# Performance work log

Measured on AMD Instinct MI355X. Metric: run time of the kernel, lower is better.

The kernel has to match this reference:

```python
import jax, jax.numpy as jnp
import numpy as np

B, S, H = 32, 4096, 512


def setup_inputs() -> dict:
    key = jax.random.key(0)
    k1, k2, k3, k4, k5 = jax.random.split(key, 5)
    scale = 1.0 / np.sqrt(H)
    return {
        "query": jax.random.normal(k1, (B, H), dtype=jnp.float32),
        "keys": jax.random.normal(k2, (B, S, H), dtype=jnp.float32),
        "key_mask": jnp.ones((B, S), dtype=bool),
        "Wq": jax.random.uniform(k3, (H, H), jnp.float32, -scale, scale),
        "Wk": jax.random.uniform(k4, (H, H), jnp.float32, -scale, scale),
        "v": jax.random.uniform(k5, (H,), jnp.float32, -scale, scale),
    }


def reference(query, keys, key_mask, Wq, Wk, v):
    # Additive (Bahdanau) attention.
    # nn.Linear(x) = x @ W.T
    q = query @ Wq.T                       # [B, H]
    k = keys @ Wk.T                        # [B, S, H]
    scores = jnp.einsum('bsh,h->bs', jnp.tanh(q[:, None, :] + k), v)  # [B, S]
    scores = jnp.where(key_mask, scores, -1e9)
    attn = jax.nn.softmax(scores, axis=-1)  # [B, S]
    ctx = jnp.einsum('bs,bsh->bh', attn, keys)  # [B, H]
    return (ctx, attn)
```

## Files before the change

kernel.cpp:

```cpp
#include <hip/hip_runtime.h>
#include <hip/hip_bf16.h>
#include <cstdint>

#define B_ 32
#define S_ 4096
#define H_ 512

typedef _Float16 f16x8 __attribute__((ext_vector_type(8)));
typedef _Float16 f16x4 __attribute__((ext_vector_type(4)));
typedef float    f32x4 __attribute__((ext_vector_type(4)));

#define GLDS16(gsrc, ldst) \
    __builtin_amdgcn_global_load_lds((const __attribute__((address_space(1))) void*)(gsrc), \
        (__attribute__((address_space(3))) void*)(ldst), 16, 0, 0)

__device__ __forceinline__ float tanh_fast(float x) {
    float e = __expf(2.0f * x);
    return 1.0f - 2.0f / (e + 1.0f);
}

__global__ void prep_q(const float* __restrict__ query,
                       const float* __restrict__ Wq,
                       float* __restrict__ q_ws) {
    int blk = blockIdx.x;
    int b   = blk >> 3;
    int r0  = (blk & 7) * 64;
    int t   = threadIdx.x;
    __shared__ float qs[H_];
    qs[t]       = query[b * H_ + t];
    qs[t + 256] = query[b * H_ + t + 256];
    __syncthreads();
    int row  = r0 + (t >> 2);
    int part = t & 3;
    const float4* wrow = (const float4*)(Wq + (size_t)row * H_) + part * 32;
    const float*  qsp  = qs + part * 128;
    float acc = 0.f;
    #pragma unroll 8
    for (int j = 0; j < 32; ++j) {
        float4 w = wrow[j];
        acc += qsp[j*4+0]*w.x + qsp[j*4+1]*w.y + qsp[j*4+2]*w.z + qsp[j*4+3]*w.w;
    }
    acc += __shfl_xor(acc, 1);
    acc += __shfl_xor(acc, 2);
    if (part == 0) q_ws[b * H_ + row] = acc;
}

__global__ void prep_wk(const float* __restrict__ Wk, _Float16* __restrict__ wk16) {
    int tid = blockIdx.x * 256 + threadIdx.x;
    int c  = tid & 3;
    int i  = (tid >> 2) & 511;
    int ks = tid >> 11;
    const float* src = Wk + (size_t)i * H_ + ks * 32 + c * 8;
    float4 a = *(const float4*)(src);
    float4 d = *(const float4*)(src + 4);
    f16x8 p;
    p[0] = (_Float16)a.x; p[1] = (_Float16)a.y; p[2] = (_Float16)a.z; p[3] = (_Float16)a.w;
    p[4] = (_Float16)d.x; p[5] = (_Float16)d.y; p[6] = (_Float16)d.z; p[7] = (_Float16)d.w;
    int swz = c ^ ((i >> 1) & 3);
    *(f16x8*)(wk16 + (size_t)ks * 16384 + i * 32 + swz * 8) = p;
}

__global__ __launch_bounds__(256, 2) void scores_kernel(
        const float* __restrict__ keys, const _Float16* __restrict__ wk16,
        const float* __restrict__ q_ws, const float* __restrict__ v,
        float* __restrict__ scores) {
    __shared__ __align__(16) _Float16 As[2][64 * 32];
    __shared__ __align__(16) _Float16 Bs[2][512 * 32];
    __shared__ float srow[4][64];

    int t    = threadIdx.x;
    int lane = t & 63;
    int wid  = t >> 6;
    int m0   = blockIdx.x * 64;
    int b    = m0 >> 12;
    const float* akeys = keys + (size_t)m0 * H_;

    f32x4 acc[4][8] = {};

    int arow0 = t >> 3, ac4 = t & 7;
    int arow1 = arow0 + 32;
    int aswz0 = (ac4 >> 1) ^ ((arow0 >> 1) & 3);
    int aswz1 = (ac4 >> 1) ^ ((arow1 >> 1) & 3);

    {
        const _Float16* bsrc = wk16;
        #pragma unroll
        for (int j = 0; j < 8; ++j)
            GLDS16(bsrc + (j * 256 + t) * 8, &Bs[0][(j * 256 + t) * 8]);
        float4 kv0 = *(const float4*)(akeys + (size_t)arow0 * H_ + ac4 * 4);
        float4 kv1 = *(const float4*)(akeys + (size_t)arow1 * H_ + ac4 * 4);
        f16x4 h0, h1;
        h0[0] = (_Float16)kv0.x; h0[1] = (_Float16)kv0.y; h0[2] = (_Float16)kv0.z; h0[3] = (_Float16)kv0.w;
        h1[0] = (_Float16)kv1.x; h1[1] = (_Float16)kv1.y; h1[2] = (_Float16)kv1.z; h1[3] = (_Float16)kv1.w;
        *(f16x4*)&As[0][arow0 * 32 + aswz0 * 8 + (ac4 & 1) * 4] = h0;
        *(f16x4*)&As[0][arow1 * 32 + aswz1 * 8 + (ac4 & 1) * 4] = h1;
    }
    __syncthreads();

    int cur = 0;
    for (int ks = 0; ks < 16; ++ks) {
        int nb = cur ^ 1;
        float4 kv0, kv1;
        if (ks < 15) {
            const _Float16* bsrc = wk16 + (size_t)(ks + 1) * 16384;
            #pragma unroll
            for (int j = 0; j < 8; ++j)
                GLDS16(bsrc + (j * 256 + t) * 8, &Bs[nb][(j * 256 + t) * 8]);
            kv0 = *(const float4*)(akeys + (size_t)arow0 * H_ + (ks + 1) * 32 + ac4 * 4);
            kv1 = *(const float4*)(akeys + (size_t)arow1 * H_ + (ks + 1) * 32 + ac4 * 4);
        }
        int chunk = lane >> 4;
        f16x8 af[4];
        #pragma unroll
        for (int mf = 0; mf < 4; ++mf) {
            int row = mf * 16 + (lane & 15);
            af[mf] = *(const f16x8*)&As[cur][row * 32 + (chunk ^ ((row >> 1) & 3)) * 8];
        }
        f16x8 bf[8];
        #pragma unroll
        for (int nf = 0; nf < 8; ++nf) {
            int row = wid * 128 + nf * 16 + (lane & 15);
            bf[nf] = *(const f16x8*)&Bs[cur][row * 32 + (chunk ^ ((row >> 1) & 3)) * 8];
        }
        #pragma unroll
        for (int mf = 0; mf < 4; ++mf)
            #pragma unroll
            for (int nf = 0; nf < 8; ++nf)
                acc[mf][nf] = __builtin_amdgcn_mfma_f32_16x16x32_f16(af[mf], bf[nf], acc[mf][nf], 0, 0, 0);
        if (ks < 15) {
            f16x4 h0, h1;
            h0[0] = (_Float16)kv0.x; h0[1] = (_Float16)kv0.y; h0[2] = (_Float16)kv0.z; h0[3] = (_Float16)kv0.w;
            h1[0] = (_Float16)kv1.x; h1[1] = (_Float16)kv1.y; h1[2] = (_Float16)kv1.z; h1[3] = (_Float16)kv1.w;
            *(f16x4*)&As[nb][arow0 * 32 + aswz0 * 8 + (ac4 & 1) * 4] = h0;
            *(f16x4*)&As[nb][arow1 * 32 + aswz1 * 8 + (ac4 & 1) * 4] = h1;
        }
        __syncthreads();
        cur = nb;
    }

    float qv[8], vv[8];
    #pragma unroll
    for (int nf = 0; nf < 8; ++nf) {
        int col = wid * 128 + nf * 16 + (lane & 15);
        qv[nf] = q_ws[b * H_ + col];
        vv[nf] = v[col];
    }
    #pragma unroll
    for (int mf = 0; mf < 4; ++mf) {
        f32x4 rs = {0.f, 0.f, 0.f, 0.f};
        #pragma unroll
        for (int nf = 0; nf < 8; ++nf)
            #pragma unroll
            for (int r = 0; r < 4; ++r)
                rs[r] += tanh_fast(qv[nf] + acc[mf][nf][r]) * vv[nf];
        #pragma unroll
        for (int off = 1; off < 16; off <<= 1)
            #pragma unroll
            for (int r = 0; r < 4; ++r)
                rs[r] += __shfl_xor(rs[r], off);
        if ((lane & 15) == 0) {
            #pragma unroll
            for (int r = 0; r < 4; ++r)
                srow[wid][mf * 16 + (lane >> 4) * 4 + r] = rs[r];
        }
    }
    __syncthreads();
    if (t < 64)
        scores[m0 + t] = srow[0][t] + srow[1][t] + srow[2][t] + srow[3][t];
}

__global__ void softmax_kernel(const float* __restrict__ scores,
                               const int* __restrict__ mask,
                               float* __restrict__ attn) {
    int b = blockIdx.x, t = threadIdx.x;
    __shared__ float red[8];
    float x[16];
    float m = -1e30f;
    #pragma unroll
    for (int j = 0; j < 16; ++j) {
        int s = t + j * 256;
        float sc = scores[b * S_ + s];
        x[j] = (mask[b * S_ + s] != 0) ? sc : -1e9f;
        m = fmaxf(m, x[j]);
    }
    #pragma unroll
    for (int off = 1; off < 64; off <<= 1) m = fmaxf(m, __shfl_xor(m, off));
    if ((t & 63) == 0) red[t >> 6] = m;
    __syncthreads();
    m = fmaxf(fmaxf(red[0], red[1]), fmaxf(red[2], red[3]));
    float sum = 0.f;
    #pragma unroll
    for (int j = 0; j < 16; ++j) { x[j] = __expf(x[j] - m); sum += x[j]; }
    #pragma unroll
    for (int off = 1; off < 64; off <<= 1) sum += __shfl_xor(sum, off);
    if ((t & 63) == 0) red[4 + (t >> 6)] = sum;
    __syncthreads();
    float inv = 1.0f / (red[4] + red[5] + red[6] + red[7]);
    #pragma unroll
    for (int j = 0; j < 16; ++j)
        attn[b * S_ + t + j * 256] = x[j] * inv;
}

__global__ void ctx_kernel(const float* __restrict__ keys,
                           const float* __restrict__ attn,
                           float* __restrict__ ctx) {
    int blk = blockIdx.x;
    int b = blk >> 4, c = blk & 15;
    int s0 = c * 256;
    int t = threadIdx.x;
    __shared__ float attn_s[256];
    __shared__ float ctx_l[512];
    attn_s[t] = attn[b * S_ + s0 + t];
    __syncthreads();
    int h4 = t & 127, sp = t >> 7;
    f32x4 acc = {0.f, 0.f, 0.f, 0.f};
    const float4* kb = (const float4*)(keys + ((size_t)b * S_ + s0) * H_);
    for (int it = 0; it < 128; ++it) {
        int srow = it * 2 + sp;
        float a = attn_s[srow];
        float4 kv = kb[(size_t)srow * 128 + h4];
        acc[0] += a * kv.x; acc[1] += a * kv.y; acc[2] += a * kv.z; acc[3] += a * kv.w;
    }
    if (sp == 0) {
        #pragma unroll
        for (int r = 0; r < 4; ++r) ctx_l[h4 * 4 + r] = acc[r];
    }
    __syncthreads();
    if (sp == 1) {
        #pragma unroll
        for (int r = 0; r < 4; ++r) ctx_l[h4 * 4 + r] += acc[r];
    }
    __syncthreads();
    atomicAdd(&ctx[b * H_ + t], ctx_l[t]);
    atomicAdd(&ctx[b * H_ + t + 256], ctx_l[t + 256]);
}

extern "C" void kernel_launch(void* const* d_in, const int* in_sizes, int n_in,
                              void* d_out, int out_size, void* d_ws, size_t ws_size,
                              hipStream_t stream) {
    const float* query = (const float*)d_in[0];
    const float* keys  = (const float*)d_in[1];
    const int*   mask  = (const int*)d_in[2];
    const float* Wq    = (const float*)d_in[3];
    const float* Wk    = (const float*)d_in[4];
    const float* v     = (const float*)d_in[5];

    float* out  = (float*)d_out;
    float* ctx  = out;
    float* attn = out + B_ * H_;

    char* ws = (char*)d_ws;
    float*    q_ws   = (float*)ws;
    _Float16* wk16   = (_Float16*)(ws + 65536);
    float*    scores = (float*)(ws + 65536 + 524288);

    hipMemsetAsync(ctx, 0, B_ * H_ * sizeof(float), stream);
    prep_q<<<256, 256, 0, stream>>>(query, Wq, q_ws);
    prep_wk<<<128, 256, 0, stream>>>(Wk, wk16);
    scores_kernel<<<2048, 256, 0, stream>>>(keys, wk16, q_ws, v, scores);
    softmax_kernel<<<32, 256, 0, stream>>>(scores, mask, attn);
    ctx_kernel<<<512, 256, 0, stream>>>(keys, attn, ctx);
}
```

Measured before the change: 494.6 us.

## Load Wk MFMA fragments straight from global into registers instead of LDS

Pre-lays out the fp16 Wk so each wave's MFMA B fragments are contiguous per lane, then loads them directly from global/L2 into a double-buffered register set. This drops the large Bs shared-memory buffer and its LDS writes and reads. The keys prefetch goes two steps ahead, the k-loop is fully unrolled, and the barrier waits only on lgkmcnt so global loads can stay in flight across it. In exchange, every block rereads Wk from L2 and register pressure rises, which could hurt occupancy under launch_bounds(256,2).

```diff
diff --git a/kernel.cpp b/kernel.cpp
--- a/kernel.cpp
+++ b/kernel.cpp
@@ -9,10 +9,6 @@
 typedef _Float16 f16x8 __attribute__((ext_vector_type(8)));
 typedef _Float16 f16x4 __attribute__((ext_vector_type(4)));
 typedef float    f32x4 __attribute__((ext_vector_type(4)));
-
-#define GLDS16(gsrc, ldst) \
-    __builtin_amdgcn_global_load_lds((const __attribute__((address_space(1))) void*)(gsrc), \
-        (__attribute__((address_space(3))) void*)(ldst), 16, 0, 0)
 
 __device__ __forceinline__ float tanh_fast(float x) {
     float e = __expf(2.0f * x);
@@ -46,18 +42,20 @@
 }
 
 __global__ void prep_wk(const float* __restrict__ Wk, _Float16* __restrict__ wk16) {
-    int tid = blockIdx.x * 256 + threadIdx.x;
-    int c  = tid & 3;
-    int i  = (tid >> 2) & 511;
-    int ks = tid >> 11;
-    const float* src = Wk + (size_t)i * H_ + ks * 32 + c * 8;
+    int tid  = blockIdx.x * 256 + threadIdx.x;
+    int lane = tid & 63;
+    int fb   = tid >> 6;
+    int ks   = fb >> 5;
+    int nfg  = fb & 31;
+    int i    = nfg * 16 + (lane & 15);
+    int k0   = ks * 32 + (lane >> 4) * 8;
+    const float* src = Wk + (size_t)i * H_ + k0;
     float4 a = *(const float4*)(src);
     float4 d = *(const float4*)(src + 4);
     f16x8 p;
     p[0] = (_Float16)a.x; p[1] = (_Float16)a.y; p[2] = (_Float16)a.z; p[3] = (_Float16)a.w;
     p[4] = (_Float16)d.x; p[5] = (_Float16)d.y; p[6] = (_Float16)d.z; p[7] = (_Float16)d.w;
-    int swz = c ^ ((i >> 1) & 3);
-    *(f16x8*)(wk16 + (size_t)ks * 16384 + i * 32 + swz * 8) = p;
+    *(f16x8*)(wk16 + (size_t)fb * 512 + lane * 8) = p;
 }
 
 __global__ __launch_bounds__(256, 2) void scores_kernel(
@@ -65,7 +63,6 @@
         const float* __restrict__ q_ws, const float* __restrict__ v,
         float* __restrict__ scores) {
     __shared__ __align__(16) _Float16 As[2][64 * 32];
-    __shared__ __align__(16) _Float16 Bs[2][512 * 32];
     __shared__ float srow[4][64];
 
     int t    = threadIdx.x;
@@ -81,61 +78,64 @@
     int arow1 = arow0 + 32;
     int aswz0 = (ac4 >> 1) ^ ((arow0 >> 1) & 3);
     int aswz1 = (ac4 >> 1) ^ ((arow1 >> 1) & 3);
+    _Float16* aw0[2] = { &As[0][arow0 * 32 + aswz0 * 8 + (ac4 & 1) * 4],
+                         &As[1][arow0 * 32 + aswz0 * 8 + (ac4 & 1) * 4] };
+    _Float16* aw1[2] = { &As[0][arow1 * 32 + aswz1 * 8 + (ac4 & 1) * 4],
+                         &As[1][arow1 * 32 + aswz1 * 8 + (ac4 & 1) * 4] };
+
+    const _Float16* bptr = wk16 + (size_t)(wid * 8) * 512 + lane * 8;
+
+    f16x8  bf[2][8];
+    float4 kvp[2][2];
 
     {
-        const _Float16* bsrc = wk16;
-        #pragma unroll
-        for (int j = 0; j < 8; ++j)
-            GLDS16(bsrc + (j * 256 + t) * 8, &Bs[0][(j * 256 + t) * 8]);
-        float4 kv0 = *(const float4*)(akeys + (size_t)arow0 * H_ + ac4 * 4);
-        float4 kv1 = *(const float4*)(akeys + (size_t)arow1 * H_ + ac4 * 4);
+        #pragma unroll
+        for (int nf = 0; nf < 8; ++nf)
+            bf[0][nf] = *(const f16x8*)(bptr + nf * 512);
+        float4 a0 = *(const float4*)(akeys + (size_t)arow0 * H_ + ac4 * 4);
+        float4 a1 = *(const float4*)(akeys + (size_t)arow1 * H_ + ac4 * 4);
+        kvp[1][0] = *(const float4*)(akeys + (size_t)arow0 * H_ + 32 + ac4 * 4);
+        kvp[1][1] = *(const float4*)(akeys + (size_t)arow1 * H_ + 32 + ac4 * 4);
         f16x4 h0, h1;
-        h0[0] = (_Float16)kv0.x; h0[1] = (_Float16)kv0.y; h0[2] = (_Float16)kv0.z; h0[3] = (_Float16)kv0.w;
-        h1[0] = (_Float16)kv1.x; h1[1] = (_Float16)kv1.y; h1[2] = (_Float16)kv1.z; h1[3] = (_Float16)kv1.w;
-        *(f16x4*)&As[0][arow0 * 32 + aswz0 * 8 + (ac4 & 1) * 4] = h0;
-        *(f16x4*)&As[0][arow1 * 32 + aswz1 * 8 + (ac4 & 1) * 4] = h1;
-    }
-    __syncthreads();
-
-    int cur = 0;
+        h0[0] = (_Float16)a0.x; h0[1] = (_Float16)a0.y; h0[2] = (_Float16)a0.z; h0[3] = (_Float16)a0.w;
+        h1[0] = (_Float16)a1.x; h1[1] = (_Float16)a1.y; h1[2] = (_Float16)a1.z; h1[3] = (_Float16)a1.w;
+        *(f16x4*)aw0[0] = h0;
+        *(f16x4*)aw1[0] = h1;
+    }
+    asm volatile("s_waitcnt lgkmcnt(0)\n\ts_barrier" ::: "memory");
+
+    #pragma unroll
     for (int ks = 0; ks < 16; ++ks) {
-        int nb = cur ^ 1;
-        float4 kv0, kv1;
+        if (ks < 14) {
+            kvp[ks & 1][0] = *(const float4*)(akeys + (size_t)arow0 * H_ + (ks + 2) * 32 + ac4 * 4);
+            kvp[ks & 1][1] = *(const float4*)(akeys + (size_t)arow1 * H_ + (ks + 2) * 32 + ac4 * 4);
+        }
         if (ks < 15) {
-            const _Float16* bsrc = wk16 + (size_t)(ks + 1) * 16384;
-            #pragma unroll
-            for (int j = 0; j < 8; ++j)
-                GLDS16(bsrc + (j * 256 + t) * 8, &Bs[nb][(j * 256 + t) * 8]);
-            kv0 = *(const float4*)(akeys + (size_t)arow0 * H_ + (ks + 1) * 32 + ac4 * 4);
-            kv1 = *(const float4*)(akeys + (size_t)arow1 * H_ + (ks + 1) * 32 + ac4 * 4);
+            #pragma unroll
+            for (int nf = 0; nf < 8; ++nf)
+                bf[(ks + 1) & 1][nf] = *(const f16x8*)(bptr + (size_t)(ks + 1) * 16384 + nf * 512);
         }
         int chunk = lane >> 4;
         f16x8 af[4];
         #pragma unroll
         for (int mf = 0; mf < 4; ++mf) {
             int row = mf * 16 + (lane & 15);
-            af[mf] = *(const f16x8*)&As[cur][row * 32 + (chunk ^ ((row >> 1) & 3)) * 8];
-        }
-        f16x8 bf[8];
-        #pragma unroll
-        for (int nf = 0; nf < 8; ++nf) {
-            int row = wid * 128 + nf * 16 + (lane & 15);
-            bf[nf] = *(const f16x8*)&Bs[cur][row * 32 + (chunk ^ ((row >> 1) & 3)) * 8];
+            af[mf] = *(const f16x8*)&As[ks & 1][row * 32 + (chunk ^ ((row >> 1) & 3)) * 8];
         }
         #pragma unroll
         for (int mf = 0; mf < 4; ++mf)
             #pragma unroll
             for (int nf = 0; nf < 8; ++nf)
-                acc[mf][nf] = __builtin_amdgcn_mfma_f32_16x16x32_f16(af[mf], bf[nf], acc[mf][nf], 0, 0, 0);
+                acc[mf][nf] = __builtin_amdgcn_mfma_f32_16x16x32_f16(af[mf], bf[ks & 1][nf], acc[mf][nf], 0, 0, 0);
         if (ks < 15) {
+            float4 k0 = kvp[(ks + 1) & 1][0], k1 = kvp[(ks + 1) & 1][1];
             f16x4 h0, h1;
-            h0[0] = (_Float16)kv0.x; h0[1] = (_Float16)kv0.y; h0[2] = (_Float16)kv0.z; h0[3] = (_Float16)kv0.w;
-            h1[0] = (_Float16)kv1.x; h1[1] = (_Float16)kv1.y; h1[2] = (_Float16)kv1.z; h1[3] = (_Float16)kv1.w;
-            *(f16x4*)&As[nb][arow0 * 32 + aswz0 * 8 + (ac4 & 1) * 4] = h0;
-            *(f16x4*)&As[nb][arow1 * 32 + aswz1 * 8 + (ac4 & 1) * 4] = h1;
-        }
-        __syncthreads();
-        cur = nb;
+            h0[0] = (_Float16)k0.x; h0[1] = (_Float16)k0.y; h0[2] = (_Float16)k0.z; h0[3] = (_Float16)k0.w;
+            h1[0] = (_Float16)k1.x; h1[1] = (_Float16)k1.y; h1[2] = (_Float16)k1.z; h1[3] = (_Float16)k1.w;
+            *(f16x4*)aw0[(ks + 1) & 1] = h0;
+            *(f16x4*)aw1[(ks + 1) & 1] = h1;
+        }
+        asm volatile("s_waitcnt lgkmcnt(0)\n\ts_barrier" ::: "memory");
     }
 
     float qv[8], vv[8];
```

Result: faster. 473.1 us (-4.3%).
